# Optimization experiments

Hardware: AMD Instinct MI355X
Metric: run time of the kernel (lower is better)

## Reference

```python
import jax, jax.numpy as jnp
import numpy as np

SEC = 20  # keypoints per section (hard-coded in original: i*20:(i+1)*20)


def smooth_l1(x):
    ax = jnp.abs(x)
    return jnp.where(ax < 1.0, 0.5 * x * x, ax - 0.5)


def setup_inputs() -> dict:
    key = jax.random.key(0)
    k1, k2, k3, k4 = jax.random.split(key, 4)
    B, K, NS = 8192, 400, 20
    return {
        "pred_keypoints": jax.random.normal(k1, (B, K, 3), dtype=jnp.float32),
        "gt_keypoints": jax.random.normal(k2, (B, K, 3), dtype=jnp.float32),
        "pred_section_logits": jax.random.normal(k3, (B, K, NS), dtype=jnp.float32),
        "gt_section_label": jax.random.randint(k4, (B, K), 0, NS, dtype=jnp.int64),
    }


def reference(pred_keypoints, gt_keypoints, pred_section_logits, gt_section_label):
    alpha, beta, delta, epsilon = 1.0, 4.0, 5.0, 6.0
    B, K, _ = pred_keypoints.shape
    S = K // SEC  # num sections

    keypoint_loss = jnp.mean(smooth_l1(pred_keypoints - gt_keypoints))

    # cross entropy over flattened [B*K, NS]
    logp = jax.nn.log_softmax(pred_section_logits, axis=-1)
    nll = -jnp.take_along_axis(logp, gt_section_label[..., None], axis=-1)[..., 0]
    section_loss = jnp.mean(nll)

    # per-section Procrustes alignment, batched over (B, S)
    P = pred_keypoints.reshape(B, S, SEC, 3)
    G = gt_keypoints.reshape(B, S, SEC, 3)
    Pc = P - P.mean(axis=2, keepdims=True)
    Gc = G - G.mean(axis=2, keepdims=True)
    # H = gt_centered^T @ pred_centered -> [B, S, 3, 3]
    H = jnp.einsum('bski,bskj->bsij', Gc, Pc)
    U, _, Vh = jnp.linalg.svd(H)  # torch.svd gives V with H = U diag(s) V^T; Vh = V^T
    R = jnp.einsum('bsik,bskj->bsij', U, Vh)  # U @ V^T
    P_aligned = jnp.einsum('bski,bsij->bskj', Pc, R)
    # sum of per-section means / S == overall mean (equal-size sections)
    rot_loss = jnp.mean(smooth_l1(P_aligned - Gc))

    # center alignment loss
    cent_loss = jnp.mean(smooth_l1(P.mean(axis=2) - G.mean(axis=2)))

    total = alpha * section_loss + beta * keypoint_loss + delta * rot_loss + epsilon * cent_loss
    return total
```

## Files before the change

kernel.cpp:

```cpp
#include <hip/hip_runtime.h>
#include <math.h>

static constexpr int Bn    = 8192;
static constexpr int Kn    = 400;
static constexpr int Sn    = 20;
static constexpr int NROWS = Bn * Kn;
static constexpr int NGRP  = Bn * Sn;

static constexpr int CE_BLOCKS = 2560, CE_TPB = 256, CE_RPT = 5;
static constexpr int PR_BLOCKS = 640,  PR_TPB = 256;

static constexpr int WS_CE   = 0;
static constexpr int WS_KP   = 4096;
static constexpr int WS_ROT  = 8192;
static constexpr int WS_CENT = 12288;

__device__ __forceinline__ float smooth_l1f(float x) {
    float ax = fabsf(x);
    return ax < 1.0f ? 0.5f * x * x : ax - 0.5f;
}

__global__ __launch_bounds__(256) void ce_kernel(
    const float* __restrict__ logits,
    const int*   __restrict__ labels,
    float*       __restrict__ ws)
{
    const int t = threadIdx.x;
    const size_t tid  = (size_t)blockIdx.x * CE_TPB + t;
    const size_t row0 = tid * CE_RPT;
    const float4* __restrict__ src = reinterpret_cast<const float4*>(logits) + row0 * 5;

    float acc = 0.0f;
#pragma unroll
    for (int r = 0; r < CE_RPT; r++) {
        float x[20];
#pragma unroll
        for (int i = 0; i < 5; i++) {
            float4 v = src[r * 5 + i];
            x[4*i+0] = v.x; x[4*i+1] = v.y; x[4*i+2] = v.z; x[4*i+3] = v.w;
        }
        int lab = labels[row0 + r];
        float m = x[0];
#pragma unroll
        for (int j = 1; j < 20; j++) m = fmaxf(m, x[j]);
        float se = 0.0f, xl = 0.0f;
#pragma unroll
        for (int j = 0; j < 20; j++) {
            se += __expf(x[j] - m);
            xl = (j == lab) ? x[j] : xl;
        }
        acc += __logf(se) + m - xl;
    }

#pragma unroll
    for (int o = 32; o > 0; o >>= 1) acc += __shfl_down(acc, o);
    __shared__ float sm[4];
    int lane = t & 63, wid = t >> 6;
    if (lane == 0) sm[wid] = acc;
    __syncthreads();
    if (t == 0) ws[WS_CE + blockIdx.x] = sm[0] + sm[1] + sm[2] + sm[3];
}

__global__ __launch_bounds__(256) void proc_kernel(
    const float* __restrict__ P,
    const float* __restrict__ G,
    float*       __restrict__ ws)
{
    const int t = threadIdx.x;
    const int grp = blockIdx.x * PR_TPB + t;
    const float4* __restrict__ pp = reinterpret_cast<const float4*>(P) + (size_t)grp * 15;
    const float4* __restrict__ gg = reinterpret_cast<const float4*>(G) + (size_t)grp * 15;

    float kp = 0.0f;
    float sp[3] = {0,0,0}, sg[3] = {0,0,0};
#pragma unroll
    for (int i = 0; i < 15; i++) {
        float4 a = pp[i], b = gg[i];
        float av[4] = {a.x, a.y, a.z, a.w};
        float bv[4] = {b.x, b.y, b.z, b.w};
#pragma unroll
        for (int j = 0; j < 4; j++) {
            int c = (4*i + j) % 3;
            kp += smooth_l1f(av[j] - bv[j]);
            sp[c] += av[j]; sg[c] += bv[j];
        }
    }
    const float inv20 = 1.0f / 20.0f;
    float mp[3] = {sp[0]*inv20, sp[1]*inv20, sp[2]*inv20};
    float mg[3] = {sg[0]*inv20, sg[1]*inv20, sg[2]*inv20};
    float cent = smooth_l1f(mp[0]-mg[0]) + smooth_l1f(mp[1]-mg[1]) + smooth_l1f(mp[2]-mg[2]);

    float X[3][3] = {{0,0,0},{0,0,0},{0,0,0}};
#pragma unroll
    for (int ch = 0; ch < 5; ch++) {
        float4 a0 = pp[3*ch+0], a1 = pp[3*ch+1], a2 = pp[3*ch+2];
        float4 b0 = gg[3*ch+0], b1 = gg[3*ch+1], b2 = gg[3*ch+2];
        float pv[12] = {a0.x,a0.y,a0.z,a0.w, a1.x,a1.y,a1.z,a1.w, a2.x,a2.y,a2.z,a2.w};
        float gv[12] = {b0.x,b0.y,b0.z,b0.w, b1.x,b1.y,b1.z,b1.w, b2.x,b2.y,b2.z,b2.w};
#pragma unroll
        for (int q = 0; q < 4; q++) {
            float pc0 = pv[3*q+0]-mp[0], pc1 = pv[3*q+1]-mp[1], pc2 = pv[3*q+2]-mp[2];
            float gc0 = gv[3*q+0]-mg[0], gc1 = gv[3*q+1]-mg[1], gc2 = gv[3*q+2]-mg[2];
            X[0][0] += gc0*pc0; X[0][1] += gc0*pc1; X[0][2] += gc0*pc2;
            X[1][0] += gc1*pc0; X[1][1] += gc1*pc1; X[1][2] += gc1*pc2;
            X[2][0] += gc2*pc0; X[2][1] += gc2*pc1; X[2][2] += gc2*pc2;
        }
    }

#pragma unroll
    for (int it = 0; it < 8; it++) {
        float c00 =  X[1][1]*X[2][2] - X[1][2]*X[2][1];
        float c01 = -(X[1][0]*X[2][2] - X[1][2]*X[2][0]);
        float c02 =  X[1][0]*X[2][1] - X[1][1]*X[2][0];
        float c10 = -(X[0][1]*X[2][2] - X[0][2]*X[2][1]);
        float c11 =  X[0][0]*X[2][2] - X[0][2]*X[2][0];
        float c12 = -(X[0][0]*X[2][1] - X[0][1]*X[2][0]);
        float c20 =  X[0][1]*X[1][2] - X[0][2]*X[1][1];
        float c21 = -(X[0][0]*X[1][2] - X[0][2]*X[1][0]);
        float c22 =  X[0][0]*X[1][1] - X[0][1]*X[1][0];
        float d = X[0][0]*c00 + X[0][1]*c01 + X[0][2]*c02;
        float ad = fmaxf(fabsf(d), 1e-30f);
        float gam = __powf(ad, -(1.0f/3.0f));
        float dsn = (d < 0.0f) ? -ad : ad;
        float k1 = 0.5f * gam;
        float k2 = 0.5f / (gam * dsn);
        X[0][0] = k1*X[0][0] + k2*c00;  X[0][1] = k1*X[0][1] + k2*c01;  X[0][2] = k1*X[0][2] + k2*c02;
        X[1][0] = k1*X[1][0] + k2*c10;  X[1][1] = k1*X[1][1] + k2*c11;  X[1][2] = k1*X[1][2] + k2*c12;
        X[2][0] = k1*X[2][0] + k2*c20;  X[2][1] = k1*X[2][1] + k2*c21;  X[2][2] = k1*X[2][2] + k2*c22;
    }
    float s9 = X[0][0]+X[0][1]+X[0][2]+X[1][0]+X[1][1]+X[1][2]+X[2][0]+X[2][1]+X[2][2];
    if (!(s9 == s9) || fabsf(s9) > 1e10f) {
        X[0][0]=1; X[0][1]=0; X[0][2]=0;
        X[1][0]=0; X[1][1]=1; X[1][2]=0;
        X[2][0]=0; X[2][1]=0; X[2][2]=1;
    }

    float rot = 0.0f;
#pragma unroll
    for (int ch = 0; ch < 5; ch++) {
        float4 a0 = pp[3*ch+0], a1 = pp[3*ch+1], a2 = pp[3*ch+2];
        float4 b0 = gg[3*ch+0], b1 = gg[3*ch+1], b2 = gg[3*ch+2];
        float pv[12] = {a0.x,a0.y,a0.z,a0.w, a1.x,a1.y,a1.z,a1.w, a2.x,a2.y,a2.z,a2.w};
        float gv[12] = {b0.x,b0.y,b0.z,b0.w, b1.x,b1.y,b1.z,b1.w, b2.x,b2.y,b2.z,b2.w};
#pragma unroll
        for (int q = 0; q < 4; q++) {
            float pc0 = pv[3*q+0]-mp[0], pc1 = pv[3*q+1]-mp[1], pc2 = pv[3*q+2]-mp[2];
            float gc0 = gv[3*q+0]-mg[0], gc1 = gv[3*q+1]-mg[1], gc2 = gv[3*q+2]-mg[2];
            float a0r = pc0*X[0][0] + pc1*X[1][0] + pc2*X[2][0] - gc0;
            float a1r = pc0*X[0][1] + pc1*X[1][1] + pc2*X[2][1] - gc1;
            float a2r = pc0*X[0][2] + pc1*X[1][2] + pc2*X[2][2] - gc2;
            rot += smooth_l1f(a0r) + smooth_l1f(a1r) + smooth_l1f(a2r);
        }
    }

#pragma unroll
    for (int o = 32; o > 0; o >>= 1) {
        kp   += __shfl_down(kp, o);
        rot  += __shfl_down(rot, o);
        cent += __shfl_down(cent, o);
    }
    __shared__ float sm[3][4];
    int lane = t & 63, wid = t >> 6;
    if (lane == 0) { sm[0][wid] = kp; sm[1][wid] = rot; sm[2][wid] = cent; }
    __syncthreads();
    if (t == 0) {
        ws[WS_KP   + blockIdx.x] = sm[0][0] + sm[0][1] + sm[0][2] + sm[0][3];
        ws[WS_ROT  + blockIdx.x] = sm[1][0] + sm[1][1] + sm[1][2] + sm[1][3];
        ws[WS_CENT + blockIdx.x] = sm[2][0] + sm[2][1] + sm[2][2] + sm[2][3];
    }
}

__global__ __launch_bounds__(256) void reduce_kernel(
    const float* __restrict__ ws, float* __restrict__ out)
{
    const int t = threadIdx.x;
    float s_ce = 0, s_kp = 0, s_rot = 0, s_cent = 0;
    for (int i = t; i < CE_BLOCKS; i += 256) s_ce += ws[WS_CE + i];
    for (int i = t; i < PR_BLOCKS; i += 256) {
        s_kp   += ws[WS_KP + i];
        s_rot  += ws[WS_ROT + i];
        s_cent += ws[WS_CENT + i];
    }
#pragma unroll
    for (int o = 32; o > 0; o >>= 1) {
        s_ce   += __shfl_down(s_ce, o);
        s_kp   += __shfl_down(s_kp, o);
        s_rot  += __shfl_down(s_rot, o);
        s_cent += __shfl_down(s_cent, o);
    }
    __shared__ float sm[4][4];
    int lane = t & 63, wid = t >> 6;
    if (lane == 0) { sm[0][wid]=s_ce; sm[1][wid]=s_kp; sm[2][wid]=s_rot; sm[3][wid]=s_cent; }
    __syncthreads();
    if (t == 0) {
        float ce   = (sm[0][0]+sm[0][1]+sm[0][2]+sm[0][3]) * (1.0f / (float)NROWS);
        float kp   = (sm[1][0]+sm[1][1]+sm[1][2]+sm[1][3]) * (1.0f / (float)(NROWS * 3));
        float rot  = (sm[2][0]+sm[2][1]+sm[2][2]+sm[2][3]) * (1.0f / (float)(NROWS * 3));
        float cent = (sm[3][0]+sm[3][1]+sm[3][2]+sm[3][3]) * (1.0f / (float)(NGRP * 3));
        out[0] = ce + 4.0f * kp + 5.0f * rot + 6.0f * cent;
    }
}

extern "C" void kernel_launch(void* const* d_in, const int* in_sizes, int n_in,
                              void* d_out, int out_size, void* d_ws, size_t ws_size,
                              hipStream_t stream) {
    const float* pred_kp = (const float*)d_in[0];
    const float* gt_kp   = (const float*)d_in[1];
    const float* logits  = (const float*)d_in[2];
    const int*   labels  = (const int*)d_in[3];
    float* out = (float*)d_out;
    float* ws  = (float*)d_ws;

    ce_kernel<<<CE_BLOCKS, CE_TPB, 0, stream>>>(logits, labels, ws);
    proc_kernel<<<PR_BLOCKS, PR_TPB, 0, stream>>>(pred_kp, gt_kp, ws);
    reduce_kernel<<<1, 256, 0, stream>>>(ws, out);
}
```

Baseline: 469.1 us.

## Fuse cross-entropy and Procrustes kernels into one interleaved launch

Merges the cross-entropy kernel and the per-section Procrustes kernel into a single launch. Block IDs are interleaved four CE blocks to one Procrustes block, so both workloads run together across the GPU. This removes one kernel launch and the tail/drain gap between the two kernels, and it lets the memory-bound CE work overlap the compute-heavy SVD iterations. The fused kernel needs as many registers as the heavier Procrustes path, which may lower occupancy for the CE blocks.

Result: faster. 451.9 us (-3.7%).

```diff
diff --git a/kernel.cpp b/kernel.cpp
--- a/kernel.cpp
+++ b/kernel.cpp
@@ -9,6 +9,7 @@
 
 static constexpr int CE_BLOCKS = 2560, CE_TPB = 256, CE_RPT = 5;
 static constexpr int PR_BLOCKS = 640,  PR_TPB = 256;
+static constexpr int FUSED_BLOCKS = CE_BLOCKS + PR_BLOCKS;
 
 static constexpr int WS_CE   = 0;
 static constexpr int WS_KP   = 4096;
@@ -20,54 +21,56 @@
     return ax < 1.0f ? 0.5f * x * x : ax - 0.5f;
 }
 
-__global__ __launch_bounds__(256) void ce_kernel(
+__global__ __launch_bounds__(256) void fused_kernel(
     const float* __restrict__ logits,
     const int*   __restrict__ labels,
-    float*       __restrict__ ws)
-{
-    const int t = threadIdx.x;
-    const size_t tid  = (size_t)blockIdx.x * CE_TPB + t;
-    const size_t row0 = tid * CE_RPT;
-    const float4* __restrict__ src = reinterpret_cast<const float4*>(logits) + row0 * 5;
-
-    float acc = 0.0f;
-#pragma unroll
-    for (int r = 0; r < CE_RPT; r++) {
-        float x[20];
-#pragma unroll
-        for (int i = 0; i < 5; i++) {
-            float4 v = src[r * 5 + i];
-            x[4*i+0] = v.x; x[4*i+1] = v.y; x[4*i+2] = v.z; x[4*i+3] = v.w;
-        }
-        int lab = labels[row0 + r];
-        float m = x[0];
-#pragma unroll
-        for (int j = 1; j < 20; j++) m = fmaxf(m, x[j]);
-        float se = 0.0f, xl = 0.0f;
-#pragma unroll
-        for (int j = 0; j < 20; j++) {
-            se += __expf(x[j] - m);
-            xl = (j == lab) ? x[j] : xl;
-        }
-        acc += __logf(se) + m - xl;
-    }
-
-#pragma unroll
-    for (int o = 32; o > 0; o >>= 1) acc += __shfl_down(acc, o);
-    __shared__ float sm[4];
-    int lane = t & 63, wid = t >> 6;
-    if (lane == 0) sm[wid] = acc;
-    __syncthreads();
-    if (t == 0) ws[WS_CE + blockIdx.x] = sm[0] + sm[1] + sm[2] + sm[3];
-}
-
-__global__ __launch_bounds__(256) void proc_kernel(
     const float* __restrict__ P,
     const float* __restrict__ G,
     float*       __restrict__ ws)
 {
-    const int t = threadIdx.x;
-    const int grp = blockIdx.x * PR_TPB + t;
+    const int t   = threadIdx.x;
+    const int bid = blockIdx.x;
+    const int lane = t & 63, wid = t >> 6;
+    __shared__ float sm[3][4];
+
+    if ((bid % 5) != 4) {
+        const int cb = (bid / 5) * 4 + (bid % 5);
+        const size_t tid  = (size_t)cb * CE_TPB + t;
+        const size_t row0 = tid * CE_RPT;
+        const float4* __restrict__ src = reinterpret_cast<const float4*>(logits) + row0 * 5;
+
+        float acc = 0.0f;
+#pragma unroll
+        for (int r = 0; r < CE_RPT; r++) {
+            float x[20];
+#pragma unroll
+            for (int i = 0; i < 5; i++) {
+                float4 v = src[r * 5 + i];
+                x[4*i+0] = v.x; x[4*i+1] = v.y; x[4*i+2] = v.z; x[4*i+3] = v.w;
+            }
+            int lab = labels[row0 + r];
+            float m = x[0];
+#pragma unroll
+            for (int j = 1; j < 20; j++) m = fmaxf(m, x[j]);
+            float se = 0.0f, xl = 0.0f;
+#pragma unroll
+            for (int j = 0; j < 20; j++) {
+                se += __expf(x[j] - m);
+                xl = (j == lab) ? x[j] : xl;
+            }
+            acc += __logf(se) + m - xl;
+        }
+
+#pragma unroll
+        for (int o = 32; o > 0; o >>= 1) acc += __shfl_down(acc, o);
+        if (lane == 0) sm[0][wid] = acc;
+        __syncthreads();
+        if (t == 0) ws[WS_CE + cb] = sm[0][0] + sm[0][1] + sm[0][2] + sm[0][3];
+        return;
+    }
+
+    const int pb  = bid / 5;
+    const int grp = pb * PR_TPB + t;
     const float4* __restrict__ pp = reinterpret_cast<const float4*>(P) + (size_t)grp * 15;
     const float4* __restrict__ gg = reinterpret_cast<const float4*>(G) + (size_t)grp * 15;
 
@@ -159,14 +162,12 @@
         rot  += __shfl_down(rot, o);
         cent += __shfl_down(cent, o);
     }
-    __shared__ float sm[3][4];
-    int lane = t & 63, wid = t >> 6;
     if (lane == 0) { sm[0][wid] = kp; sm[1][wid] = rot; sm[2][wid] = cent; }
     __syncthreads();
     if (t == 0) {
-        ws[WS_KP   + blockIdx.x] = sm[0][0] + sm[0][1] + sm[0][2] + sm[0][3];
-        ws[WS_ROT  + blockIdx.x] = sm[1][0] + sm[1][1] + sm[1][2] + sm[1][3];
-        ws[WS_CENT + blockIdx.x] = sm[2][0] + sm[2][1] + sm[2][2] + sm[2][3];
+        ws[WS_KP   + pb] = sm[0][0] + sm[0][1] + sm[0][2] + sm[0][3];
+        ws[WS_ROT  + pb] = sm[1][0] + sm[1][1] + sm[1][2] + sm[1][3];
+        ws[WS_CENT + pb] = sm[2][0] + sm[2][1] + sm[2][2] + sm[2][3];
     }
 }
 
@@ -211,7 +212,6 @@
     float* out = (float*)d_out;
     float* ws  = (float*)d_ws;
 
-    ce_kernel<<<CE_BLOCKS, CE_TPB, 0, stream>>>(logits, labels, ws);
-    proc_kernel<<<PR_BLOCKS, PR_TPB, 0, stream>>>(pred_kp, gt_kp, ws);
+    fused_kernel<<<FUSED_BLOCKS, 256, 0, stream>>>(logits, labels, pred_kp, gt_kp, ws);
     reduce_kernel<<<1, 256, 0, stream>>>(ws, out);
 }
```
